# Optimization experiments

Hardware: AMD Instinct MI355X
Metric: run time of the kernel (lower is better)

## Reference

```python
import jax, jax.numpy as jnp
import numpy as np

B, T_IN, T_DEC = 64, 64, 47   # batch, encoder len, decoder steps (max_length_output-1)
V, E, H = 32000, 512, 1024    # vocab, embed dim, hidden


def setup_inputs() -> dict:
    key = jax.random.key(0)
    ks = jax.random.split(key, 12)
    s = 0.02
    return {
        "tokens": jax.random.randint(ks[0], (B, T_DEC), 0, V),
        "memory": jax.random.normal(ks[1], (B, T_IN, H), jnp.float32),
        "enc_h": jax.random.normal(ks[2], (B, H), jnp.float32),
        "enc_c": jax.random.normal(ks[3], (B, H), jnp.float32),
        "emb": jax.random.normal(ks[4], (V, E), jnp.float32) * s,
        "Wm": jax.random.normal(ks[5], (H, H), jnp.float32) * s,      # Luong memory_layer (no bias)
        "Wa": jax.random.normal(ks[6], (2 * H, H), jnp.float32) * s,  # attention_layer (no bias)
        "lstm_k": jax.random.normal(ks[7], (E + H, 4 * H), jnp.float32) * s,
        "lstm_r": jax.random.normal(ks[8], (H, 4 * H), jnp.float32) * s,
        "lstm_b": jnp.zeros((4 * H,), jnp.float32),
        "fc_w": jax.random.normal(ks[9], (H, V), jnp.float32) * s,
        "fc_b": jnp.zeros((V,), jnp.float32),
    }


def reference(tokens, memory, enc_h, enc_c, emb, Wm, Wa, lstm_k, lstm_r, lstm_b, fc_w, fc_b):
    # Luong attention keys: memory projected once, outside the decode loop
    keys_att = jnp.einsum('bth,hu->btu', memory, Wm)          # [B,T_in,H]
    xs = jnp.swapaxes(emb[tokens], 0, 1)                      # [T_dec,B,E] teacher-forced inputs

    def step(carry, x_t):
        h, c, attn = carry
        # AttentionWrapper: cell input = concat(embedding, prev attention)
        inp = jnp.concatenate([x_t, attn], axis=-1)           # [B,E+H]
        z = inp @ lstm_k + h @ lstm_r + lstm_b                # [B,4H], Keras gate order i,f,g,o
        i, f, g, o = jnp.split(z, 4, axis=-1)
        c2 = jax.nn.sigmoid(f) * c + jax.nn.sigmoid(i) * jnp.tanh(g)
        h2 = jax.nn.sigmoid(o) * jnp.tanh(c2)
        # Luong score = query . keys; full-length memory (no mask needed)
        score = jnp.einsum('bh,bth->bt', h2, keys_att)        # [B,T_in]
        align = jax.nn.softmax(score, axis=-1)
        ctx = jnp.einsum('bt,bth->bh', align, memory)         # [B,H]
        attn2 = jnp.concatenate([h2, ctx], axis=-1) @ Wa      # attention_layer -> [B,H]
        logits = attn2 @ fc_w + fc_b                          # output_layer -> [B,V]
        return (h2, c2, attn2), logits

    init = (enc_h, enc_c, jnp.zeros_like(enc_h))
    _, ys = jax.lax.scan(step, init, xs)                      # [T_dec,B,V]
    return jnp.swapaxes(ys, 0, 1)                             # [B,T_dec,V]
```

## Files before the change

### kernel.cpp

```cpp
#include <hip/hip_runtime.h>

typedef __bf16 bf16;
typedef __bf16 bf16x8 __attribute__((ext_vector_type(8)));
typedef __bf16 bf16x4 __attribute__((ext_vector_type(4)));
typedef float  f32x4  __attribute__((ext_vector_type(4)));

__device__ __forceinline__ void async16(const bf16* g, bf16* l) {
  __builtin_amdgcn_global_load_lds(
      (__attribute__((address_space(1))) void*)(void*)(const_cast<bf16*>(g)),
      (__attribute__((address_space(3))) void*)(void*)l,
      16, 0, 0);
}


__global__ void cvt_bf16(const float* __restrict__ s, bf16* __restrict__ d, int n) {
  int i = blockIdx.x * blockDim.x + threadIdx.x;
  int stride = gridDim.x * blockDim.x;
  for (int k = i; k < n; k += stride) d[k] = (bf16)s[k];
}

__global__ void transpose_to_bf16(const float* __restrict__ src, bf16* __restrict__ dst,
                                  int R, int C) {
  __shared__ float tile[32][33];
  int c0 = blockIdx.x * 32, r0 = blockIdx.y * 32;
  int tx = threadIdx.x, ty = threadIdx.y;
#pragma unroll
  for (int k = 0; k < 32; k += 8)
    tile[ty + k][tx] = src[(size_t)(r0 + ty + k) * C + (c0 + tx)];
  __syncthreads();
#pragma unroll
  for (int k = 0; k < 32; k += 8)
    dst[(size_t)(c0 + ty + k) * R + (r0 + tx)] = (bf16)tile[tx][ty + k];
}

__global__ void gather_emb(const int* __restrict__ tokens, const float* __restrict__ emb,
                           bf16* __restrict__ X) {
  int r = blockIdx.x;
  int tid = threadIdx.x;
  if (r < 3008) {
    int t = r >> 6, b = r & 63;
    int tok = tokens[b * 47 + t];
    const float* e = emb + (size_t)tok * 512;
    for (int k = tid; k < 512; k += 128) X[(size_t)r * 512 + k] = (bf16)e[k];
  } else {
    for (int k = tid; k < 512; k += 128) X[(size_t)r * 512 + k] = (bf16)0.f;
  }
}

__global__ void init_state(const float* __restrict__ enc_h, const float* __restrict__ enc_c,
                           bf16* __restrict__ S0, float* __restrict__ cbuf) {
  int i = blockIdx.x * 256 + threadIdx.x;
  int b = i >> 10, u = i & 1023;
  S0[(size_t)b * 2048 + u]        = (bf16)enc_h[i];
  S0[(size_t)b * 2048 + 1024 + u] = (bf16)0.f;
  cbuf[i] = enc_c[i];
}

template <int MODE>
__global__ __launch_bounds__(256) void gemm_bt(
    const bf16* __restrict__ A, int lda,
    const bf16* __restrict__ B, int ldb, int K,
    void* __restrict__ C, int ldc,
    const void* __restrict__ aux) {
  __shared__ bf16 As[128 * 32];
  __shared__ bf16 Bs[128 * 32];
  const int tid = threadIdx.x;
  const int wave = tid >> 6, lane = tid & 63;
  const int wm = wave >> 1, wn = wave & 1;
  const int quad = lane >> 4, l16 = lane & 15;
  const size_t r0 = (size_t)blockIdx.y * 128;
  const size_t c0 = (size_t)blockIdx.x * 128;

  f32x4 acc[4][4] = {};

  for (int k0 = 0; k0 < K; k0 += 32) {
#pragma unroll
    for (int j = 0; j < 2; ++j) {
      int seg = j * 256 + tid;
      int row = seg >> 2, ks = seg & 3;
      async16(A + (r0 + row) * (size_t)lda + k0 + ks * 8, As + seg * 8);
    }
#pragma unroll
    for (int j = 0; j < 2; ++j) {
      int seg = j * 256 + tid;
      int row = seg >> 2, ks = seg & 3;
      async16(B + (c0 + row) * (size_t)ldb + k0 + ks * 8, Bs + seg * 8);
    }
    __syncthreads();
    bf16x8 af[4], bfr[4];
#pragma unroll
    for (int mi = 0; mi < 4; ++mi)
      af[mi] = *(const bf16x8*)(As + (wm * 64 + mi * 16 + l16) * 32 + quad * 8);
#pragma unroll
    for (int ni = 0; ni < 4; ++ni)
      bfr[ni] = *(const bf16x8*)(Bs + (wn * 64 + ni * 16 + l16) * 32 + quad * 8);
#pragma unroll
    for (int mi = 0; mi < 4; ++mi)
#pragma unroll
      for (int ni = 0; ni < 4; ++ni)
        acc[mi][ni] = __builtin_amdgcn_mfma_f32_16x16x32_bf16(af[mi], bfr[ni], acc[mi][ni], 0, 0, 0);
    __syncthreads();
  }

#pragma unroll
  for (int mi = 0; mi < 4; ++mi)
#pragma unroll
    for (int ni = 0; ni < 4; ++ni)
#pragma unroll
      for (int reg = 0; reg < 4; ++reg) {
        size_t r = r0 + wm * 64 + mi * 16 + quad * 4 + reg;
        size_t c = c0 + wn * 64 + ni * 16 + l16;
        float v = acc[mi][ni][reg];
        if (MODE == 0) {
          ((bf16*)C)[r * ldc + c] = (bf16)v;
        } else if (MODE == 1) {
          if (c < 1024) v += (float)((const bf16*)aux)[r * 1024 + c];
          ((bf16*)C)[r * ldc + c] = (bf16)v;
        } else if (MODE == 2) {
          v += ((const float*)aux)[c];
          ((float*)C)[r * ldc + c] = v;
        } else if (MODE == 3) {
          if (r < 3008) {
            size_t t = r >> 6, b = r & 63;
            ((float*)C)[(b * 47 + t) * (size_t)32000 + c] = v + ((const float*)aux)[c];
          }
        } else {
          ((float*)C)[r * ldc + c] = v;
        }
      }
}

__global__ __launch_bounds__(128) void step_gates(
    const bf16* __restrict__ Sin,
    const bf16* __restrict__ Bt,
    int ldb, int K,
    const float* __restrict__ precomp_t,
    float* __restrict__ cbuf,
    bf16* __restrict__ Sout,
    bf16* __restrict__ HC_t)
{
  __shared__ bf16 As[64 * 32];
  __shared__ bf16 Bs[32 * 32];
  __shared__ float zs[64 * 32];
  const int tid = threadIdx.x;
  const int wave = tid >> 6, lane = tid & 63;
  const int quad = lane >> 4, l16 = lane & 15;
  const int p = blockIdx.x;

  f32x4 acc[4] = {};

  for (int k0 = 0; k0 < K; k0 += 32) {
#pragma unroll
    for (int j = 0; j < 2; ++j) {
      int seg = j * 128 + tid;
      int row = seg >> 2, ks = seg & 3;
      async16(Sin + (size_t)row * 2048 + k0 + ks * 8, As + seg * 8);
    }
    {
      int nl = tid >> 2, ks = tid & 3;
      int gate = nl >> 3, s = nl & 7;
      int ng = gate * 1024 + p * 8 + s;
      async16(Bt + (size_t)ng * ldb + k0 + ks * 8, Bs + tid * 8);
    }
    __syncthreads();
    bf16x8 bfr = *(const bf16x8*)(Bs + (wave * 16 + l16) * 32 + quad * 8);
#pragma unroll
    for (int mi = 0; mi < 4; ++mi) {
      bf16x8 afr = *(const bf16x8*)(As + (mi * 16 + l16) * 32 + quad * 8);
      acc[mi] = __builtin_amdgcn_mfma_f32_16x16x32_bf16(afr, bfr, acc[mi], 0, 0, 0);
    }
    __syncthreads();
  }

  {
    int nl = wave * 16 + l16;
    int gate = nl >> 3, s = nl & 7;
#pragma unroll
    for (int mi = 0; mi < 4; ++mi)
#pragma unroll
      for (int reg = 0; reg < 4; ++reg) {
        int row = mi * 16 + quad * 4 + reg;
        float z = acc[mi][reg] + precomp_t[(size_t)row * 4096 + gate * 1024 + p * 8 + s];
        zs[row * 32 + nl] = z;
      }
  }
  __syncthreads();

#pragma unroll
  for (int ii = 0; ii < 4; ++ii) {
    int idx = ii * 128 + tid;
    int b = idx >> 3, s2 = idx & 7;
    int j = p * 8 + s2;
    float iv = zs[b * 32 + s2];
    float fv = zs[b * 32 + 8 + s2];
    float gv = zs[b * 32 + 16 + s2];
    float ov = zs[b * 32 + 24 + s2];
    float c_old = cbuf[b * 1024 + j];
    float ig = 1.f / (1.f + __expf(-iv));
    float fg = 1.f / (1.f + __expf(-fv));
    float og = 1.f / (1.f + __expf(-ov));
    float c2 = fg * c_old + ig * tanhf(gv);
    float h2 = og * tanhf(c2);
    cbuf[b * 1024 + j] = c2;
    bf16 hb = (bf16)h2;
    Sout[(size_t)b * 2048 + j] = hb;
    HC_t[(size_t)b * 2048 + j] = hb;
  }
}

__global__ __launch_bounds__(256) void step_attn(
    const bf16* __restrict__ Sh,
    const float* __restrict__ keys,
    const bf16* __restrict__ memB,
    bf16* __restrict__ HC_t)
{
  __shared__ float h2s[1024];
  __shared__ float sm[64];
  const int b = blockIdx.x;
  const int tid = threadIdx.x;
  const int wave = tid >> 6, lane = tid & 63;

#pragma unroll
  for (int j = 0; j < 4; ++j) {
    int u = j * 256 + tid;
    h2s[u] = (float)Sh[(size_t)b * 2048 + u];
  }
  __syncthreads();

  for (int ii = 0; ii < 16; ++ii) {
    int it = wave * 16 + ii;
    const float* krow = keys + ((size_t)b * 64 + it) * 1024;
    float pr = 0.f;
#pragma unroll
    for (int q = 0; q < 16; ++q) {
      int u = q * 64 + lane;
      pr += h2s[u] * krow[u];
    }
#pragma unroll
    for (int off = 32; off > 0; off >>= 1) pr += __shfl_xor(pr, off);
    if (lane == 0) sm[it] = pr;
  }
  __syncthreads();

  if (tid < 64) {
    float s = sm[tid];
    float mx = s;
#pragma unroll
    for (int off = 32; off > 0; off >>= 1) mx = fmaxf(mx, __shfl_xor(mx, off));
    float e = __expf(s - mx);
    float sum = e;
#pragma unroll
    for (int off = 32; off > 0; off >>= 1) sum += __shfl_xor(sum, off);
    sm[tid] = e / sum;
  }
  __syncthreads();

  int u0 = tid * 4;
  float a0 = 0.f, a1 = 0.f, a2 = 0.f, a3 = 0.f;
  for (int i = 0; i < 64; ++i) {
    float al = sm[i];
    bf16x4 m4 = *(const bf16x4*)(memB + ((size_t)b * 64 + i) * 1024 + u0);
    a0 += al * (float)m4[0];
    a1 += al * (float)m4[1];
    a2 += al * (float)m4[2];
    a3 += al * (float)m4[3];
  }
  bf16* so = (bf16*)Sh;
  so[(size_t)b * 2048 + 1024 + u0 + 0] = (bf16)a0;
  so[(size_t)b * 2048 + 1024 + u0 + 1] = (bf16)a1;
  so[(size_t)b * 2048 + 1024 + u0 + 2] = (bf16)a2;
  so[(size_t)b * 2048 + 1024 + u0 + 3] = (bf16)a3;
  HC_t[(size_t)b * 2048 + 1024 + u0 + 0] = (bf16)a0;
  HC_t[(size_t)b * 2048 + 1024 + u0 + 1] = (bf16)a1;
  HC_t[(size_t)b * 2048 + 1024 + u0 + 2] = (bf16)a2;
  HC_t[(size_t)b * 2048 + 1024 + u0 + 3] = (bf16)a3;
}


extern "C" void kernel_launch(void* const* d_in, const int* in_sizes, int n_in,
                              void* d_out, int out_size, void* d_ws, size_t ws_size,
                              hipStream_t stream) {
  const int*   tokens = (const int*)d_in[0];
  const float* memory = (const float*)d_in[1];
  const float* enc_h  = (const float*)d_in[2];
  const float* enc_c  = (const float*)d_in[3];
  const float* emb    = (const float*)d_in[4];
  const float* Wm     = (const float*)d_in[5];
  const float* Wa     = (const float*)d_in[6];
  const float* lstm_k = (const float*)d_in[7];
  const float* lstm_r = (const float*)d_in[8];
  const float* lstm_b = (const float*)d_in[9];
  const float* fc_w   = (const float*)d_in[10];
  const float* fc_b   = (const float*)d_in[11];
  float* out = (float*)d_out;

  char* ob = (char*)d_out;
  size_t off = 0;
  auto alloc_o = [&](size_t bytes) { char* q = ob + off; off += bytes; return q; };
  bf16*  memB    = (bf16*)alloc_o(8388608);
  float* keys    = (float*)alloc_o(16777216);
  bf16*  WaB     = (bf16*)alloc_o(4194304);
  bf16*  WmT     = (bf16*)alloc_o(2097152);
  bf16*  KpT     = (bf16*)alloc_o(8388608);
  bf16*  KxT     = (bf16*)alloc_o(4194304);
  bf16*  RT      = (bf16*)alloc_o(8388608);
  bf16*  WaT     = (bf16*)alloc_o(4194304);
  bf16*  X       = (bf16*)alloc_o(3145728);
  bf16*  W12T    = (bf16*)alloc_o(16777216);
  bf16*  S0      = (bf16*)alloc_o(262144);
  bf16*  S1      = (bf16*)alloc_o(262144);
  float* cbuf    = (float*)alloc_o(262144);
  bf16*  HC      = (bf16*)alloc_o(12582912);
  float* precomp = (float*)alloc_o(50331648);

  char* wb = (char*)d_ws;
  bf16* fcwT  = (bf16*)(wb);
  bf16* attnb = (bf16*)(wb + 65536000);

  dim3 tb(32, 8);

  cvt_bf16<<<2048, 256, 0, stream>>>(memory, memB, 4194304);
  cvt_bf16<<<2048, 256, 0, stream>>>(Wa, WaB, 2097152);
  transpose_to_bf16<<<dim3(32, 32), tb, 0, stream>>>(Wm, WmT, 1024, 1024);
  transpose_to_bf16<<<dim3(128, 32), tb, 0, stream>>>(lstm_k + (size_t)512 * 4096, KpT, 1024, 4096);
  transpose_to_bf16<<<dim3(128, 16), tb, 0, stream>>>(lstm_k, KxT, 512, 4096);
  transpose_to_bf16<<<dim3(128, 32), tb, 0, stream>>>(lstm_r, RT, 1024, 4096);
  transpose_to_bf16<<<dim3(32, 64), tb, 0, stream>>>(Wa, WaT, 2048, 1024);
  transpose_to_bf16<<<dim3(1000, 32), tb, 0, stream>>>(fc_w, fcwT, 1024, 32000);
  gather_emb<<<3072, 128, 0, stream>>>(tokens, emb, X);
  init_state<<<256, 256, 0, stream>>>(enc_h, enc_c, S0, cbuf);

  gemm_bt<4><<<dim3(8, 32), 256, 0, stream>>>(memB, 1024, WmT, 1024, 1024, keys, 1024, nullptr);
  gemm_bt<1><<<dim3(16, 32), 256, 0, stream>>>(KpT, 1024, WaB, 1024, 1024, W12T, 2048, RT);
  gemm_bt<2><<<dim3(32, 24), 256, 0, stream>>>(X, 512, KxT, 512, 512, precomp, 4096, lstm_b);

  for (int t = 0; t < 47; ++t) {
    const bf16* Sin = (t & 1) ? S1 : S0;
    bf16* Sout = (t & 1) ? S0 : S1;
    const bf16* Bt = (t == 0) ? RT : W12T;
    int ldb = (t == 0) ? 1024 : 2048;
    int K = (t == 0) ? 1024 : 2048;
    bf16* HC_t = HC + (size_t)t * 64 * 2048;
    step_gates<<<128, 128, 0, stream>>>(Sin, Bt, ldb, K,
                                        precomp + (size_t)t * 64 * 4096, cbuf, Sout, HC_t);
    step_attn<<<64, 256, 0, stream>>>(Sout, keys, memB, HC_t);
  }

  gemm_bt<0><<<dim3(8, 24), 256, 0, stream>>>(HC, 2048, WaT, 2048, 2048, attnb, 1024, nullptr);
  gemm_bt<3><<<dim3(250, 24), 256, 0, stream>>>(attnb, 1024, fcwT, 1024, 1024, out, 32000, fc_b);

  (void)in_sizes; (void)n_in; (void)out_size; (void)ws_size;
}
```

Measured before the change: 2.905 ms.

## Replace per-step decoder launches with persistent cooperative kernel using grid sync

Fuses the 94 per-timestep gate and attention kernel launches into one cooperative persistent kernel of 128 blocks that loops over all 47 steps with grid-wide barriers. Each block keeps its 32-column slice of the fused recurrent weight matrix resident in LDS (128 KB, XOR-swizzled) and holds the cell state in registers instead of a global buffer. State is read directly from the previous step's HC slice, which removes the ping-pong buffers. This trades launch overhead and repeated weight streaming for two grid syncs per step, and attention runs on only 64 of the 128 blocks.

```diff
diff --git a/kernel.cpp b/kernel.cpp
--- a/kernel.cpp
+++ b/kernel.cpp
@@ -1,4 +1,7 @@
 #include <hip/hip_runtime.h>
+#include <hip/hip_cooperative_groups.h>
+
+namespace cg = cooperative_groups;
 
 typedef __bf16 bf16;
 typedef __bf16 bf16x8 __attribute__((ext_vector_type(8)));
@@ -47,13 +50,11 @@
   }
 }
 
-__global__ void init_state(const float* __restrict__ enc_h, const float* __restrict__ enc_c,
-                           bf16* __restrict__ S0, float* __restrict__ cbuf) {
+__global__ void init_state(const float* __restrict__ enc_h, bf16* __restrict__ S0) {
   int i = blockIdx.x * 256 + threadIdx.x;
   int b = i >> 10, u = i & 1023;
   S0[(size_t)b * 2048 + u]        = (bf16)enc_h[i];
   S0[(size_t)b * 2048 + 1024 + u] = (bf16)0.f;
-  cbuf[i] = enc_c[i];
 }
 
 template <int MODE>
@@ -130,150 +131,166 @@
       }
 }
 
-__global__ __launch_bounds__(128) void step_gates(
-    const bf16* __restrict__ Sin,
-    const bf16* __restrict__ Bt,
-    int ldb, int K,
-    const float* __restrict__ precomp_t,
-    float* __restrict__ cbuf,
-    bf16* __restrict__ Sout,
-    bf16* __restrict__ HC_t)
+__global__ __launch_bounds__(256, 1) void decoder_persistent(
+    const bf16* __restrict__ S0,
+    const bf16* __restrict__ W12T,
+    const bf16* __restrict__ RT,
+    const float* __restrict__ precomp,
+    const float* __restrict__ enc_c,
+    const float* __restrict__ keys,
+    const bf16* __restrict__ memB,
+    bf16* __restrict__ HC)
 {
-  __shared__ bf16 As[64 * 32];
-  __shared__ bf16 Bs[32 * 32];
-  __shared__ float zs[64 * 32];
+  __shared__ bf16 Bsm[32 * 2048];
+  __shared__ float scratch[2048];
+
   const int tid = threadIdx.x;
+  const int p = blockIdx.x;
   const int wave = tid >> 6, lane = tid & 63;
   const int quad = lane >> 4, l16 = lane & 15;
-  const int p = blockIdx.x;
-
-  f32x4 acc[4] = {};
-
-  for (int k0 = 0; k0 < K; k0 += 32) {
-#pragma unroll
-    for (int j = 0; j < 2; ++j) {
-      int seg = j * 128 + tid;
-      int row = seg >> 2, ks = seg & 3;
-      async16(Sin + (size_t)row * 2048 + k0 + ks * 8, As + seg * 8);
-    }
-    {
-      int nl = tid >> 2, ks = tid & 3;
-      int gate = nl >> 3, s = nl & 7;
-      int ng = gate * 1024 + p * 8 + s;
-      async16(Bt + (size_t)ng * ldb + k0 + ks * 8, Bs + tid * 8);
-    }
+  const int wm = wave >> 1, wn = wave & 1;
+  const int n_l = wn * 16 + l16;
+  const int bswz = (n_l & 7) << 4;
+  const int growB = (n_l >> 3) * 1024 + p * 8 + (n_l & 7);
+
+  for (int slot = tid; slot < 8192; slot += 256) {
+    int nl = slot >> 8;
+    int kbs = (slot & 255) * 16;
+    int gkb = kbs ^ ((nl & 7) << 4);
+    int grow = (nl >> 3) * 1024 + p * 8 + (nl & 7);
+    bf16x8 v = *(const bf16x8*)((const char*)W12T + (size_t)grow * 4096 + gkb);
+    *(bf16x8*)((char*)Bsm + nl * 4096 + kbs) = v;
+  }
+
+  float c_reg[2];
+#pragma unroll
+  for (int ii = 0; ii < 2; ++ii) {
+    int idx = ii * 256 + tid;
+    int b = idx >> 3, s2 = idx & 7;
+    c_reg[ii] = enc_c[b * 1024 + p * 8 + s2];
+  }
+
+  cg::grid_group grid = cg::this_grid();
+  __syncthreads();
+
+  for (int t = 0; t < 47; ++t) {
+    const bf16* Sin = (t == 0) ? S0 : (HC + (size_t)(t - 1) * 131072);
+    bf16* HC_t = HC + (size_t)t * 131072;
+    const float* pct = precomp + (size_t)t * 64 * 4096;
+
+    f32x4 acc[2] = {};
+    const bf16* a0 = Sin + (size_t)(wm * 32 + l16) * 2048 + quad * 8;
+    const bf16* a1 = a0 + (size_t)16 * 2048;
+    if (t == 0) {
+      const bf16* brow = RT + (size_t)growB * 1024 + quad * 8;
+#pragma unroll 8
+      for (int ks = 0; ks < 32; ++ks) {
+        bf16x8 bfr = *(const bf16x8*)(brow + ks * 32);
+        bf16x8 af0 = *(const bf16x8*)(a0 + ks * 32);
+        bf16x8 af1 = *(const bf16x8*)(a1 + ks * 32);
+        acc[0] = __builtin_amdgcn_mfma_f32_16x16x32_bf16(af0, bfr, acc[0], 0, 0, 0);
+        acc[1] = __builtin_amdgcn_mfma_f32_16x16x32_bf16(af1, bfr, acc[1], 0, 0, 0);
+      }
+    } else {
+      const char* bbase = (const char*)Bsm + n_l * 4096;
+#pragma unroll 8
+      for (int ks = 0; ks < 64; ++ks) {
+        bf16x8 bfr = *(const bf16x8*)(bbase + ((ks * 64 + quad * 16) ^ bswz));
+        bf16x8 af0 = *(const bf16x8*)(a0 + ks * 32);
+        bf16x8 af1 = *(const bf16x8*)(a1 + ks * 32);
+        acc[0] = __builtin_amdgcn_mfma_f32_16x16x32_bf16(af0, bfr, acc[0], 0, 0, 0);
+        acc[1] = __builtin_amdgcn_mfma_f32_16x16x32_bf16(af1, bfr, acc[1], 0, 0, 0);
+      }
+    }
+
+#pragma unroll
+    for (int mi = 0; mi < 2; ++mi)
+#pragma unroll
+      for (int reg = 0; reg < 4; ++reg) {
+        int row = wm * 32 + mi * 16 + quad * 4 + reg;
+        scratch[row * 32 + n_l] = acc[mi][reg]
+            + pct[(size_t)row * 4096 + (n_l >> 3) * 1024 + p * 8 + (n_l & 7)];
+      }
     __syncthreads();
-    bf16x8 bfr = *(const bf16x8*)(Bs + (wave * 16 + l16) * 32 + quad * 8);
-#pragma unroll
-    for (int mi = 0; mi < 4; ++mi) {
-      bf16x8 afr = *(const bf16x8*)(As + (mi * 16 + l16) * 32 + quad * 8);
-      acc[mi] = __builtin_amdgcn_mfma_f32_16x16x32_bf16(afr, bfr, acc[mi], 0, 0, 0);
-    }
-    __syncthreads();
-  }
-
-  {
-    int nl = wave * 16 + l16;
-    int gate = nl >> 3, s = nl & 7;
-#pragma unroll
-    for (int mi = 0; mi < 4; ++mi)
-#pragma unroll
-      for (int reg = 0; reg < 4; ++reg) {
-        int row = mi * 16 + quad * 4 + reg;
-        float z = acc[mi][reg] + precomp_t[(size_t)row * 4096 + gate * 1024 + p * 8 + s];
-        zs[row * 32 + nl] = z;
-      }
-  }
-  __syncthreads();
-
-#pragma unroll
-  for (int ii = 0; ii < 4; ++ii) {
-    int idx = ii * 128 + tid;
-    int b = idx >> 3, s2 = idx & 7;
-    int j = p * 8 + s2;
-    float iv = zs[b * 32 + s2];
-    float fv = zs[b * 32 + 8 + s2];
-    float gv = zs[b * 32 + 16 + s2];
-    float ov = zs[b * 32 + 24 + s2];
-    float c_old = cbuf[b * 1024 + j];
-    float ig = 1.f / (1.f + __expf(-iv));
-    float fg = 1.f / (1.f + __expf(-fv));
-    float og = 1.f / (1.f + __expf(-ov));
-    float c2 = fg * c_old + ig * tanhf(gv);
-    float h2 = og * tanhf(c2);
-    cbuf[b * 1024 + j] = c2;
-    bf16 hb = (bf16)h2;
-    Sout[(size_t)b * 2048 + j] = hb;
-    HC_t[(size_t)b * 2048 + j] = hb;
-  }
-}
-
-__global__ __launch_bounds__(256) void step_attn(
-    const bf16* __restrict__ Sh,
-    const float* __restrict__ keys,
-    const bf16* __restrict__ memB,
-    bf16* __restrict__ HC_t)
-{
-  __shared__ float h2s[1024];
-  __shared__ float sm[64];
-  const int b = blockIdx.x;
-  const int tid = threadIdx.x;
-  const int wave = tid >> 6, lane = tid & 63;
-
-#pragma unroll
-  for (int j = 0; j < 4; ++j) {
-    int u = j * 256 + tid;
-    h2s[u] = (float)Sh[(size_t)b * 2048 + u];
-  }
-  __syncthreads();
-
-  for (int ii = 0; ii < 16; ++ii) {
-    int it = wave * 16 + ii;
-    const float* krow = keys + ((size_t)b * 64 + it) * 1024;
-    float pr = 0.f;
-#pragma unroll
-    for (int q = 0; q < 16; ++q) {
-      int u = q * 64 + lane;
-      pr += h2s[u] * krow[u];
-    }
-#pragma unroll
-    for (int off = 32; off > 0; off >>= 1) pr += __shfl_xor(pr, off);
-    if (lane == 0) sm[it] = pr;
-  }
-  __syncthreads();
-
-  if (tid < 64) {
-    float s = sm[tid];
-    float mx = s;
-#pragma unroll
-    for (int off = 32; off > 0; off >>= 1) mx = fmaxf(mx, __shfl_xor(mx, off));
-    float e = __expf(s - mx);
-    float sum = e;
-#pragma unroll
-    for (int off = 32; off > 0; off >>= 1) sum += __shfl_xor(sum, off);
-    sm[tid] = e / sum;
-  }
-  __syncthreads();
-
-  int u0 = tid * 4;
-  float a0 = 0.f, a1 = 0.f, a2 = 0.f, a3 = 0.f;
-  for (int i = 0; i < 64; ++i) {
-    float al = sm[i];
-    bf16x4 m4 = *(const bf16x4*)(memB + ((size_t)b * 64 + i) * 1024 + u0);
-    a0 += al * (float)m4[0];
-    a1 += al * (float)m4[1];
-    a2 += al * (float)m4[2];
-    a3 += al * (float)m4[3];
-  }
-  bf16* so = (bf16*)Sh;
-  so[(size_t)b * 2048 + 1024 + u0 + 0] = (bf16)a0;
-  so[(size_t)b * 2048 + 1024 + u0 + 1] = (bf16)a1;
-  so[(size_t)b * 2048 + 1024 + u0 + 2] = (bf16)a2;
-  so[(size_t)b * 2048 + 1024 + u0 + 3] = (bf16)a3;
-  HC_t[(size_t)b * 2048 + 1024 + u0 + 0] = (bf16)a0;
-  HC_t[(size_t)b * 2048 + 1024 + u0 + 1] = (bf16)a1;
-  HC_t[(size_t)b * 2048 + 1024 + u0 + 2] = (bf16)a2;
-  HC_t[(size_t)b * 2048 + 1024 + u0 + 3] = (bf16)a3;
+
+#pragma unroll
+    for (int ii = 0; ii < 2; ++ii) {
+      int idx = ii * 256 + tid;
+      int b = idx >> 3, s2 = idx & 7;
+      float iv = scratch[b * 32 + s2];
+      float fv = scratch[b * 32 + 8 + s2];
+      float gv = scratch[b * 32 + 16 + s2];
+      float ov = scratch[b * 32 + 24 + s2];
+      float ig = 1.f / (1.f + __expf(-iv));
+      float fg = 1.f / (1.f + __expf(-fv));
+      float og = 1.f / (1.f + __expf(-ov));
+      float c2 = fg * c_reg[ii] + ig * tanhf(gv);
+      float h2 = og * tanhf(c2);
+      c_reg[ii] = c2;
+      HC_t[(size_t)b * 2048 + p * 8 + s2] = (bf16)h2;
+    }
+    __threadfence();
+    grid.sync();
+    __threadfence();
+
+    if (p < 64) {
+      const int b = p;
+      float* h2s = scratch;
+      float* sm = scratch + 1024;
+#pragma unroll
+      for (int jj = 0; jj < 4; ++jj) {
+        int u = jj * 256 + tid;
+        h2s[u] = (float)HC_t[(size_t)b * 2048 + u];
+      }
+      __syncthreads();
+
+      for (int ii = 0; ii < 16; ++ii) {
+        int it = wave * 16 + ii;
+        const float* krow = keys + ((size_t)b * 64 + it) * 1024;
+        float pr = 0.f;
+#pragma unroll
+        for (int q = 0; q < 16; ++q) {
+          int u = q * 64 + lane;
+          pr += h2s[u] * krow[u];
+        }
+#pragma unroll
+        for (int off = 32; off > 0; off >>= 1) pr += __shfl_xor(pr, off);
+        if (lane == 0) sm[it] = pr;
+      }
+      __syncthreads();
+
+      if (tid < 64) {
+        float s = sm[tid];
+        float mx = s;
+#pragma unroll
+        for (int off = 32; off > 0; off >>= 1) mx = fmaxf(mx, __shfl_xor(mx, off));
+        float e = __expf(s - mx);
+        float sum = e;
+#pragma unroll
+        for (int off = 32; off > 0; off >>= 1) sum += __shfl_xor(sum, off);
+        sm[tid] = e / sum;
+      }
+      __syncthreads();
+
+      int u0 = tid * 4;
+      float a0c = 0.f, a1c = 0.f, a2c = 0.f, a3c = 0.f;
+      for (int i = 0; i < 64; ++i) {
+        float al = sm[i];
+        bf16x4 m4 = *(const bf16x4*)(memB + ((size_t)b * 64 + i) * 1024 + u0);
+        a0c += al * (float)m4[0];
+        a1c += al * (float)m4[1];
+        a2c += al * (float)m4[2];
+        a3c += al * (float)m4[3];
+      }
+      HC_t[(size_t)b * 2048 + 1024 + u0 + 0] = (bf16)a0c;
+      HC_t[(size_t)b * 2048 + 1024 + u0 + 1] = (bf16)a1c;
+      HC_t[(size_t)b * 2048 + 1024 + u0 + 2] = (bf16)a2c;
+      HC_t[(size_t)b * 2048 + 1024 + u0 + 3] = (bf16)a3c;
+    }
+    __threadfence();
+    grid.sync();
+    __threadfence();
+  }
 }
 
 
@@ -308,8 +325,6 @@
   bf16*  X       = (bf16*)alloc_o(3145728);
   bf16*  W12T    = (bf16*)alloc_o(16777216);
   bf16*  S0      = (bf16*)alloc_o(262144);
-  bf16*  S1      = (bf16*)alloc_o(262144);
-  float* cbuf    = (float*)alloc_o(262144);
   bf16*  HC      = (bf16*)alloc_o(12582912);
   float* precomp = (float*)alloc_o(50331648);
 
@@ -328,22 +343,25 @@
   transpose_to_bf16<<<dim3(32, 64), tb, 0, stream>>>(Wa, WaT, 2048, 1024);
   transpose_to_bf16<<<dim3(1000, 32), tb, 0, stream>>>(fc_w, fcwT, 1024, 32000);
   gather_emb<<<3072, 128, 0, stream>>>(tokens, emb, X);
-  init_state<<<256, 256, 0, stream>>>(enc_h, enc_c, S0, cbuf);
+  init_state<<<256, 256, 0, stream>>>(enc_h, S0);
 
   gemm_bt<4><<<dim3(8, 32), 256, 0, stream>>>(memB, 1024, WmT, 1024, 1024, keys, 1024, nullptr);
   gemm_bt<1><<<dim3(16, 32), 256, 0, stream>>>(KpT, 1024, WaB, 1024, 1024, W12T, 2048, RT);
   gemm_bt<2><<<dim3(32, 24), 256, 0, stream>>>(X, 512, KxT, 512, 512, precomp, 4096, lstm_b);
 
-  for (int t = 0; t < 47; ++t) {
-    const bf16* Sin = (t & 1) ? S1 : S0;
-    bf16* Sout = (t & 1) ? S0 : S1;
-    const bf16* Bt = (t == 0) ? RT : W12T;
-    int ldb = (t == 0) ? 1024 : 2048;
-    int K = (t == 0) ? 1024 : 2048;
-    bf16* HC_t = HC + (size_t)t * 64 * 2048;
-    step_gates<<<128, 128, 0, stream>>>(Sin, Bt, ldb, K,
-                                        precomp + (size_t)t * 64 * 4096, cbuf, Sout, HC_t);
-    step_attn<<<64, 256, 0, stream>>>(Sout, keys, memB, HC_t);
+  {
+    const bf16* S0c = S0;
+    const bf16* W12Tc = W12T;
+    const bf16* RTc = RT;
+    const float* precompc = precomp;
+    const float* enc_cc = enc_c;
+    const float* keysc = keys;
+    const bf16* memBc = memB;
+    bf16* HCc = HC;
+    void* kargs[] = { (void*)&S0c, (void*)&W12Tc, (void*)&RTc, (void*)&precompc,
+                      (void*)&enc_cc, (void*)&keysc, (void*)&memBc, (void*)&HCc };
+    hipLaunchCooperativeKernel((void*)decoder_persistent, dim3(128), dim3(256),
+                               kargs, 0, stream);
   }
 
   gemm_bt<0><<<dim3(8, 24), 256, 0, stream>>>(HC, 2048, WaT, 2048, 2048, attnb, 1024, nullptr);
```

Result: slower. 6.447 ms (+121.9%).

## Restructure recurrent step kernels with full-K LDS weight slab and direct HC reuse

Applied to the files above, without the earlier changes.

The per-step gate kernel now loads each block's full 16-column weight slab (all of K) into LDS in one shot with an XOR swizzle and reads A directly from global. It launches 256 blocks of 256 threads instead of looping over K tiles with a sync on every iteration. The attention kernel keeps h in registers and uses vectorized key loads. The state ping-pong buffers are dropped in favour of reading the previous HC slice. The final vocab GEMM swaps its grid axes so that blocks sharing an fc_w column tile run adjacently, which may improve L2 reuse. The large LDS footprint (64KB) limits occupancy per CU.

```diff
diff --git a/kernel.cpp b/kernel.cpp
--- a/kernel.cpp
+++ b/kernel.cpp
@@ -56,7 +56,7 @@
   cbuf[i] = enc_c[i];
 }
 
-template <int MODE>
+template <int MODE, int SWAP = 0>
 __global__ __launch_bounds__(256) void gemm_bt(
     const bf16* __restrict__ A, int lda,
     const bf16* __restrict__ B, int ldb, int K,
@@ -68,8 +68,8 @@
   const int wave = tid >> 6, lane = tid & 63;
   const int wm = wave >> 1, wn = wave & 1;
   const int quad = lane >> 4, l16 = lane & 15;
-  const size_t r0 = (size_t)blockIdx.y * 128;
-  const size_t c0 = (size_t)blockIdx.x * 128;
+  const size_t r0 = (size_t)(SWAP ? blockIdx.x : blockIdx.y) * 128;
+  const size_t c0 = (size_t)(SWAP ? blockIdx.y : blockIdx.x) * 128;
 
   f32x4 acc[4][4] = {};
 
@@ -130,71 +130,68 @@
       }
 }
 
-__global__ __launch_bounds__(128) void step_gates(
+template <int KK>
+__global__ __launch_bounds__(256) void step_gates2(
     const bf16* __restrict__ Sin,
     const bf16* __restrict__ Bt,
-    int ldb, int K,
-    const float* __restrict__ precomp_t,
+    int ldb,
+    const float* __restrict__ pct,
     float* __restrict__ cbuf,
-    bf16* __restrict__ Sout,
     bf16* __restrict__ HC_t)
 {
-  __shared__ bf16 As[64 * 32];
-  __shared__ bf16 Bs[32 * 32];
-  __shared__ float zs[64 * 32];
+  __shared__ bf16 Bs[16 * 2048];
+  __shared__ float zs[64 * 16];
   const int tid = threadIdx.x;
+  const int p = blockIdx.x;
   const int wave = tid >> 6, lane = tid & 63;
   const int quad = lane >> 4, l16 = lane & 15;
-  const int p = blockIdx.x;
-
-  f32x4 acc[4] = {};
-
-  for (int k0 = 0; k0 < K; k0 += 32) {
-#pragma unroll
-    for (int j = 0; j < 2; ++j) {
-      int seg = j * 128 + tid;
-      int row = seg >> 2, ks = seg & 3;
-      async16(Sin + (size_t)row * 2048 + k0 + ks * 8, As + seg * 8);
+
+  constexpr int NSEG = KK / 8;
+  constexpr int SH = (KK == 2048) ? 8 : 7;
+#pragma unroll
+  for (int i = 0; i < 16 * NSEG / 256; ++i) {
+    int seg = i * 256 + tid;
+    int n = seg >> SH;
+    int ko = seg & (NSEG - 1);
+    int gkb = (ko * 16) ^ ((n & 7) << 4);
+    int ng = (n >> 2) * 1024 + p * 4 + (n & 3);
+    async16(Bt + (size_t)ng * ldb + (gkb >> 1), Bs + n * 2048 + ko * 8);
+  }
+
+  const bf16* arow = Sin + (size_t)(wave * 16 + l16) * 2048 + quad * 8;
+  const char* bbase = (const char*)Bs + l16 * 4096;
+  const int bswz = (l16 & 7) << 4;
+  __syncthreads();
+
+  f32x4 acc0 = {}, acc1 = {};
+  constexpr int KS = KK / 32;
+#pragma unroll 8
+  for (int ks = 0; ks < KS; ks += 2) {
+    bf16x8 b0 = *(const bf16x8*)(bbase + ((ks * 64 + quad * 16) ^ bswz));
+    bf16x8 a0 = *(const bf16x8*)(arow + (size_t)ks * 32);
+    acc0 = __builtin_amdgcn_mfma_f32_16x16x32_bf16(a0, b0, acc0, 0, 0, 0);
+    bf16x8 b1 = *(const bf16x8*)(bbase + (((ks + 1) * 64 + quad * 16) ^ bswz));
+    bf16x8 a1 = *(const bf16x8*)(arow + (size_t)(ks + 1) * 32);
+    acc1 = __builtin_amdgcn_mfma_f32_16x16x32_bf16(a1, b1, acc1, 0, 0, 0);
+  }
+
+  {
+    int gcol = (l16 >> 2) * 1024 + p * 4 + (l16 & 3);
+#pragma unroll
+    for (int reg = 0; reg < 4; ++reg) {
+      int row = wave * 16 + quad * 4 + reg;
+      zs[row * 16 + l16] = acc0[reg] + acc1[reg] + pct[(size_t)row * 4096 + gcol];
     }
-    {
-      int nl = tid >> 2, ks = tid & 3;
-      int gate = nl >> 3, s = nl & 7;
-      int ng = gate * 1024 + p * 8 + s;
-      async16(Bt + (size_t)ng * ldb + k0 + ks * 8, Bs + tid * 8);
-    }
-    __syncthreads();
-    bf16x8 bfr = *(const bf16x8*)(Bs + (wave * 16 + l16) * 32 + quad * 8);
-#pragma unroll
-    for (int mi = 0; mi < 4; ++mi) {
-      bf16x8 afr = *(const bf16x8*)(As + (mi * 16 + l16) * 32 + quad * 8);
-      acc[mi] = __builtin_amdgcn_mfma_f32_16x16x32_bf16(afr, bfr, acc[mi], 0, 0, 0);
-    }
-    __syncthreads();
-  }
+  }
+  __syncthreads();
 
   {
-    int nl = wave * 16 + l16;
-    int gate = nl >> 3, s = nl & 7;
-#pragma unroll
-    for (int mi = 0; mi < 4; ++mi)
-#pragma unroll
-      for (int reg = 0; reg < 4; ++reg) {
-        int row = mi * 16 + quad * 4 + reg;
-        float z = acc[mi][reg] + precomp_t[(size_t)row * 4096 + gate * 1024 + p * 8 + s];
-        zs[row * 32 + nl] = z;
-      }
-  }
-  __syncthreads();
-
-#pragma unroll
-  for (int ii = 0; ii < 4; ++ii) {
-    int idx = ii * 128 + tid;
-    int b = idx >> 3, s2 = idx & 7;
-    int j = p * 8 + s2;
-    float iv = zs[b * 32 + s2];
-    float fv = zs[b * 32 + 8 + s2];
-    float gv = zs[b * 32 + 16 + s2];
-    float ov = zs[b * 32 + 24 + s2];
+    int b = tid >> 2, s = tid & 3;
+    int j = p * 4 + s;
+    float iv = zs[b * 16 + s];
+    float fv = zs[b * 16 + 4 + s];
+    float gv = zs[b * 16 + 8 + s];
+    float ov = zs[b * 16 + 12 + s];
     float c_old = cbuf[b * 1024 + j];
     float ig = 1.f / (1.f + __expf(-iv));
     float fg = 1.f / (1.f + __expf(-fv));
@@ -202,40 +199,41 @@
     float c2 = fg * c_old + ig * tanhf(gv);
     float h2 = og * tanhf(c2);
     cbuf[b * 1024 + j] = c2;
-    bf16 hb = (bf16)h2;
-    Sout[(size_t)b * 2048 + j] = hb;
-    HC_t[(size_t)b * 2048 + j] = hb;
-  }
-}
-
-__global__ __launch_bounds__(256) void step_attn(
-    const bf16* __restrict__ Sh,
+    HC_t[(size_t)b * 2048 + j] = (bf16)h2;
+  }
+}
+
+__global__ __launch_bounds__(256) void step_attn2(
+    bf16* __restrict__ HC_t,
     const float* __restrict__ keys,
-    const bf16* __restrict__ memB,
-    bf16* __restrict__ HC_t)
+    const bf16* __restrict__ memB)
 {
-  __shared__ float h2s[1024];
   __shared__ float sm[64];
   const int b = blockIdx.x;
   const int tid = threadIdx.x;
   const int wave = tid >> 6, lane = tid & 63;
 
-#pragma unroll
-  for (int j = 0; j < 4; ++j) {
-    int u = j * 256 + tid;
-    h2s[u] = (float)Sh[(size_t)b * 2048 + u];
-  }
-  __syncthreads();
-
+  float hv[16];
+  {
+    const bf16* hp = HC_t + (size_t)b * 2048 + lane * 16;
+    bf16x8 h0 = *(const bf16x8*)(hp);
+    bf16x8 h1 = *(const bf16x8*)(hp + 8);
+#pragma unroll
+    for (int e = 0; e < 8; ++e) { hv[e] = (float)h0[e]; hv[8 + e] = (float)h1[e]; }
+  }
+
+#pragma unroll 4
   for (int ii = 0; ii < 16; ++ii) {
     int it = wave * 16 + ii;
-    const float* krow = keys + ((size_t)b * 64 + it) * 1024;
-    float pr = 0.f;
-#pragma unroll
-    for (int q = 0; q < 16; ++q) {
-      int u = q * 64 + lane;
-      pr += h2s[u] * krow[u];
-    }
+    const float* krow = keys + ((size_t)b * 64 + it) * 1024 + lane * 16;
+    f32x4 k0 = *(const f32x4*)(krow);
+    f32x4 k1 = *(const f32x4*)(krow + 4);
+    f32x4 k2 = *(const f32x4*)(krow + 8);
+    f32x4 k3 = *(const f32x4*)(krow + 12);
+    float pr = hv[0] * k0[0] + hv[1] * k0[1] + hv[2] * k0[2] + hv[3] * k0[3]
+             + hv[4] * k1[0] + hv[5] * k1[1] + hv[6] * k1[2] + hv[7] * k1[3]
+             + hv[8] * k2[0] + hv[9] * k2[1] + hv[10] * k2[2] + hv[11] * k2[3]
+             + hv[12] * k3[0] + hv[13] * k3[1] + hv[14] * k3[2] + hv[15] * k3[3];
 #pragma unroll
     for (int off = 32; off > 0; off >>= 1) pr += __shfl_xor(pr, off);
     if (lane == 0) sm[it] = pr;
@@ -257,6 +255,7 @@
 
   int u0 = tid * 4;
   float a0 = 0.f, a1 = 0.f, a2 = 0.f, a3 = 0.f;
+#pragma unroll 4
   for (int i = 0; i < 64; ++i) {
     float al = sm[i];
     bf16x4 m4 = *(const bf16x4*)(memB + ((size_t)b * 64 + i) * 1024 + u0);
@@ -265,15 +264,11 @@
     a2 += al * (float)m4[2];
     a3 += al * (float)m4[3];
   }
-  bf16* so = (bf16*)Sh;
-  so[(size_t)b * 2048 + 1024 + u0 + 0] = (bf16)a0;
-  so[(size_t)b * 2048 + 1024 + u0 + 1] = (bf16)a1;
-  so[(size_t)b * 2048 + 1024 + u0 + 2] = (bf16)a2;
-  so[(size_t)b * 2048 + 1024 + u0 + 3] = (bf16)a3;
-  HC_t[(size_t)b * 2048 + 1024 + u0 + 0] = (bf16)a0;
-  HC_t[(size_t)b * 2048 + 1024 + u0 + 1] = (bf16)a1;
-  HC_t[(size_t)b * 2048 + 1024 + u0 + 2] = (bf16)a2;
-  HC_t[(size_t)b * 2048 + 1024 + u0 + 3] = (bf16)a3;
+  bf16* so = HC_t + (size_t)b * 2048 + 1024 + u0;
+  so[0] = (bf16)a0;
+  so[1] = (bf16)a1;
+  so[2] = (bf16)a2;
+  so[3] = (bf16)a3;
 }
 
 
@@ -308,7 +303,6 @@
   bf16*  X       = (bf16*)alloc_o(3145728);
   bf16*  W12T    = (bf16*)alloc_o(16777216);
   bf16*  S0      = (bf16*)alloc_o(262144);
-  bf16*  S1      = (bf16*)alloc_o(262144);
   float* cbuf    = (float*)alloc_o(262144);
   bf16*  HC      = (bf16*)alloc_o(12582912);
   float* precomp = (float*)alloc_o(50331648);
@@ -335,19 +329,18 @@
   gemm_bt<2><<<dim3(32, 24), 256, 0, stream>>>(X, 512, KxT, 512, 512, precomp, 4096, lstm_b);
 
   for (int t = 0; t < 47; ++t) {
-    const bf16* Sin = (t & 1) ? S1 : S0;
-    bf16* Sout = (t & 1) ? S0 : S1;
-    const bf16* Bt = (t == 0) ? RT : W12T;
-    int ldb = (t == 0) ? 1024 : 2048;
-    int K = (t == 0) ? 1024 : 2048;
-    bf16* HC_t = HC + (size_t)t * 64 * 2048;
-    step_gates<<<128, 128, 0, stream>>>(Sin, Bt, ldb, K,
-                                        precomp + (size_t)t * 64 * 4096, cbuf, Sout, HC_t);
-    step_attn<<<64, 256, 0, stream>>>(Sout, keys, memB, HC_t);
+    const bf16* Sin = (t == 0) ? S0 : (HC + (size_t)(t - 1) * 131072);
+    bf16* HC_t = HC + (size_t)t * 131072;
+    const float* pct = precomp + (size_t)t * 262144;
+    if (t == 0)
+      step_gates2<1024><<<256, 256, 0, stream>>>(Sin, RT, 1024, pct, cbuf, HC_t);
+    else
+      step_gates2<2048><<<256, 256, 0, stream>>>(Sin, W12T, 2048, pct, cbuf, HC_t);
+    step_attn2<<<64, 256, 0, stream>>>(HC_t, keys, memB);
   }
 
   gemm_bt<0><<<dim3(8, 24), 256, 0, stream>>>(HC, 2048, WaT, 2048, 2048, attnb, 1024, nullptr);
-  gemm_bt<3><<<dim3(250, 24), 256, 0, stream>>>(attnb, 1024, fcwT, 1024, 1024, out, 32000, fc_b);
+  gemm_bt<3, 1><<<dim3(24, 250), 256, 0, stream>>>(attnb, 1024, fcwT, 1024, 1024, out, 32000, fc_b);
 
   (void)in_sizes; (void)n_in; (void)out_size; (void)ws_size;
 }
```

New measurement: 2.425 ms. -16.5%, faster.
